# Kernel tuning notes

Hardware: AMD Instinct MI355X
Metric: run time of the kernel (lower is better)

The kernel has to match this reference:

```python
import jax, jax.numpy as jnp
import numpy as np

H = W = 128          # input_size
N = 128              # output_size[0] == output_size[1]
B = 64
LIN = (H - 2) * (W - 2)          # 15876
TRI = (N * N + N) // 2           # 8256
TI, TJ = np.triu_indices(N)
TI = jnp.asarray(TI); TJ = jnp.asarray(TJ)


def setup_inputs() -> dict:
    key = jax.random.key(0)
    ks = jax.random.split(key, 7)
    return {
        "x": jax.random.normal(ks[0], (B, 1, H, W), jnp.float32),
        "conv1_w": jax.random.normal(ks[1], (4, 1, 3, 3), jnp.float32) * 0.1,
        "conv1_b": jax.random.normal(ks[2], (4,), jnp.float32) * 0.1,
        "conv2_w": jax.random.normal(ks[3], (1, 4, 1, 1), jnp.float32) * 0.1,
        "conv2_b": jax.random.normal(ks[4], (1,), jnp.float32) * 0.1,
        "out_w": jax.random.normal(ks[5], (TRI, LIN), jnp.float32) * (1.0 / np.sqrt(LIN)),
        "out_b": jax.random.normal(ks[6], (TRI,), jnp.float32) * 0.01,
    }


def reference(x, conv1_w, conv1_b, conv2_w, conv2_b, out_w, out_b):
    dn = ('NCHW', 'OIHW', 'NCHW')
    # conv1 (1->4, 3x3, VALID) + relu
    h = jax.lax.conv_general_dilated(x, conv1_w, (1, 1), 'VALID', dimension_numbers=dn)
    h = jax.nn.relu(h + conv1_b[None, :, None, None])
    # conv2 (4->1, 1x1)
    h = jax.lax.conv_general_dilated(h, conv2_w, (1, 1), 'VALID', dimension_numbers=dn)
    h = h + conv2_b[None, :, None, None]
    # flatten -> linear
    h = h.reshape(x.shape[0], -1)                       # [B, LIN]
    v = h @ out_w.T + out_b                             # [B, TRI]
    # vectorized symmetric triu scatter (replaces per-sample Python loop)
    y = jnp.zeros((x.shape[0], N, N), v.dtype)
    y = y.at[:, TI, TJ].set(v).at[:, TJ, TI].set(v)
    return y[:, None, :, :]                             # [B, 1, N, N]
```

## Files before the change

kernel.cpp:

```cpp
#include <hip/hip_runtime.h>
#include <hip/hip_bf16.h>

#define H_IN   128
#define W_IN   128
#define B_SZ   64
#define CONV_O 126
#define K_DIM  15876
#define N_TRI  8256
#define N_OUT  128
#define BK     32
#define BN     64
#define NSTEPS 497
#define K8     1988
#define KSPLIT 16

typedef short  short8  __attribute__((ext_vector_type(8)));
typedef float  floatx4 __attribute__((ext_vector_type(4)));

__device__ inline short f2bf(float f) {
    union { __hip_bfloat16 h; short s; } u;
    u.h = __float2bfloat16(f);
    return u.s;
}

__global__ __launch_bounds__(256) void conv_kernel(
    const float* __restrict__ x,
    const float* __restrict__ w1,
    const float* __restrict__ b1,
    const float* __restrict__ w2,
    const float* __restrict__ b2,
    unsigned short* __restrict__ hsw)
{
    int t = blockIdx.x * 256 + threadIdx.x;
    int j  = t & 7;
    int m  = (t >> 3) & 63;
    int k8 = t >> 9;
    int p  = k8 * 8 + j;
    float val = 0.f;
    if (p < K_DIM) {
        int oy = p / CONV_O;
        int ox = p - oy * CONV_O;
        const float* xb = x + m * (H_IN * W_IN) + oy * W_IN + ox;
        float xin[9];
#pragma unroll
        for (int dy = 0; dy < 3; ++dy)
#pragma unroll
            for (int dx = 0; dx < 3; ++dx)
                xin[dy * 3 + dx] = xb[dy * W_IN + dx];
        float acc = b2[0];
#pragma unroll
        for (int c = 0; c < 4; ++c) {
            float s = b1[c];
#pragma unroll
            for (int q = 0; q < 9; ++q) s = fmaf(w1[c * 9 + q], xin[q], s);
            s = fmaxf(s, 0.f);
            acc = fmaf(w2[c], s, acc);
        }
        val = acc;
    }
    hsw[t] = (unsigned short)f2bf(val);
}

__global__ __launch_bounds__(256, 4) void gemm_kernel(
    const unsigned short* __restrict__ hsw,
    const float* __restrict__ w,
    float* __restrict__ v)
{
    __shared__ __align__(16) short Bs[64 * 40];

    const int n0    = blockIdx.x * BN;
    const int split = blockIdx.y;
    const int s0 = (NSTEPS * split) / KSPLIT;
    const int s1 = (NSTEPS * (split + 1)) / KSPLIT;

    const int t    = threadIdx.x;
    const int lane = t & 63;
    const int wv   = t >> 6;
    const int quad = lane >> 4;
    const int l16  = lane & 15;

    const int mh = (wv >> 1) * 32;
    const int nq = (wv & 1) * 32;

    const int brow = t >> 2;
    const int bk   = (t & 3) * 8;

    const int boff0 = (nq + l16) * 40 + quad * 8;
    const int boff1 = (nq + 16 + l16) * 40 + quad * 8;

    floatx4 acc00 = {0.f,0.f,0.f,0.f}, acc01 = {0.f,0.f,0.f,0.f};
    floatx4 acc10 = {0.f,0.f,0.f,0.f}, acc11 = {0.f,0.f,0.f,0.f};

    for (int s = s0; s < s1; ++s) {
        const int k0 = s * BK;

        const float* wp = w + (size_t)(n0 + brow) * K_DIM + k0 + bk;
        float bv[8];
        if (k0 + BK <= K_DIM) {
            float4 x0 = *(const float4*)wp;
            float4 x1 = *(const float4*)(wp + 4);
            bv[0]=x0.x; bv[1]=x0.y; bv[2]=x0.z; bv[3]=x0.w;
            bv[4]=x1.x; bv[5]=x1.y; bv[6]=x1.z; bv[7]=x1.w;
        } else {
#pragma unroll
            for (int q = 0; q < 8; ++q)
                bv[q] = (k0 + bk + q < K_DIM) ? wp[q] : 0.f;
        }
        short8 bs;
#pragma unroll
        for (int q = 0; q < 8; ++q) bs[q] = f2bf(bv[q]);

        __syncthreads();
        *(short8*)(Bs + brow * 40 + bk) = bs;
        __syncthreads();

        const unsigned short* ap = hsw + (size_t)(s * 4 + quad) * (64 * 8);
        short8 a0 = *(const short8*)(ap + (mh + l16) * 8);
        short8 a1 = *(const short8*)(ap + (mh + 16 + l16) * 8);
        short8 b0 = *(const short8*)(Bs + boff0);
        short8 b1 = *(const short8*)(Bs + boff1);

        acc00 = __builtin_amdgcn_mfma_f32_16x16x32_bf16(a0, b0, acc00, 0, 0, 0);
        acc01 = __builtin_amdgcn_mfma_f32_16x16x32_bf16(a0, b1, acc01, 0, 0, 0);
        acc10 = __builtin_amdgcn_mfma_f32_16x16x32_bf16(a1, b0, acc10, 0, 0, 0);
        acc11 = __builtin_amdgcn_mfma_f32_16x16x32_bf16(a1, b1, acc11, 0, 0, 0);
    }

    const int nc = n0 + nq + l16;
#pragma unroll
    for (int r = 0; r < 4; ++r) {
        int m = mh + quad * 4 + r;
        atomicAdd(&v[(size_t)m * N_TRI + nc],              acc00[r]);
        atomicAdd(&v[(size_t)m * N_TRI + nc + 16],         acc01[r]);
        atomicAdd(&v[(size_t)(m + 16) * N_TRI + nc],       acc10[r]);
        atomicAdd(&v[(size_t)(m + 16) * N_TRI + nc + 16],  acc11[r]);
    }
}

__global__ __launch_bounds__(256) void scatter_kernel(
    const float* __restrict__ v,
    const float* __restrict__ out_b,
    float* __restrict__ y)
{
    int t = blockIdx.x * 256 + threadIdx.x;
    int b  = t >> 14;
    int ij = t & 16383;
    int i = ij >> 7, j = ij & 127;
    int ii = min(i, j), jj = max(i, j);
    int tri = ii * N_OUT - ((ii * (ii - 1)) >> 1) + (jj - ii);
    y[t] = v[(size_t)b * N_TRI + tri] + out_b[tri];
}

extern "C" void kernel_launch(void* const* d_in, const int* in_sizes, int n_in,
                              void* d_out, int out_size, void* d_ws, size_t ws_size,
                              hipStream_t stream) {
    const float* x   = (const float*)d_in[0];
    const float* c1w = (const float*)d_in[1];
    const float* c1b = (const float*)d_in[2];
    const float* c2w = (const float*)d_in[3];
    const float* c2b = (const float*)d_in[4];
    const float* ow  = (const float*)d_in[5];
    const float* ob  = (const float*)d_in[6];
    float* y = (float*)d_out;

    unsigned short* hsw = (unsigned short*)d_ws;
    float* v = (float*)((char*)d_ws + (size_t)K8 * 64 * 8 * 2);

    hipMemsetAsync(v, 0, (size_t)B_SZ * N_TRI * sizeof(float), stream);

    conv_kernel<<<(K8 * 64 * 8) / 256, 256, 0, stream>>>(x, c1w, c1b, c2w, c2b, hsw);
    gemm_kernel<<<dim3(N_TRI / BN, KSPLIT), 256, 0, stream>>>(hsw, ow, v);
    scatter_kernel<<<(B_SZ * N_OUT * N_OUT) / 256, 256, 0, stream>>>(v, ob, y);
}
```

Baseline: 730.1 us.

## Double-buffer GEMM B tile with register prefetch and replace atomics with split-K reduce

The GEMM loop now prefetches the next step's fp32 weight slice and activation fragments into registers while the current step computes. It double-buffers the shared B tile so only one barrier per step is needed instead of two. Split-K partials are written with plain stores to a per-split buffer, and a new reduce kernel sums them, replacing the memset and float atomics. This adds about 34 MB of partial-buffer traffic and an extra launch in exchange for removing atomic contention and the sync stalls.

```diff
diff --git a/kernel.cpp b/kernel.cpp
--- a/kernel.cpp
+++ b/kernel.cpp
@@ -64,9 +64,9 @@
 __global__ __launch_bounds__(256, 4) void gemm_kernel(
     const unsigned short* __restrict__ hsw,
     const float* __restrict__ w,
-    float* __restrict__ v)
-{
-    __shared__ __align__(16) short Bs[64 * 40];
+    float* __restrict__ vp)
+{
+    __shared__ __align__(16) short Bs[2][64 * 40];
 
     const int n0    = blockIdx.x * BN;
     const int split = blockIdx.y;
@@ -88,14 +88,17 @@
     const int boff0 = (nq + l16) * 40 + quad * 8;
     const int boff1 = (nq + 16 + l16) * 40 + quad * 8;
 
+    const float* wrow = w + (size_t)(n0 + brow) * K_DIM + bk;
+
     floatx4 acc00 = {0.f,0.f,0.f,0.f}, acc01 = {0.f,0.f,0.f,0.f};
     floatx4 acc10 = {0.f,0.f,0.f,0.f}, acc11 = {0.f,0.f,0.f,0.f};
 
-    for (int s = s0; s < s1; ++s) {
-        const int k0 = s * BK;
-
-        const float* wp = w + (size_t)(n0 + brow) * K_DIM + k0 + bk;
-        float bv[8];
+    float  bv[8];
+    short8 a0n, a1n;
+
+    {
+        const int k0 = s0 * BK;
+        const float* wp = wrow + k0;
         if (k0 + BK <= K_DIM) {
             float4 x0 = *(const float4*)wp;
             float4 x1 = *(const float4*)(wp + 4);
@@ -106,35 +109,77 @@
             for (int q = 0; q < 8; ++q)
                 bv[q] = (k0 + bk + q < K_DIM) ? wp[q] : 0.f;
         }
-        short8 bs;
-#pragma unroll
-        for (int q = 0; q < 8; ++q) bs[q] = f2bf(bv[q]);
-
-        __syncthreads();
-        *(short8*)(Bs + brow * 40 + bk) = bs;
-        __syncthreads();
-
-        const unsigned short* ap = hsw + (size_t)(s * 4 + quad) * (64 * 8);
-        short8 a0 = *(const short8*)(ap + (mh + l16) * 8);
-        short8 a1 = *(const short8*)(ap + (mh + 16 + l16) * 8);
-        short8 b0 = *(const short8*)(Bs + boff0);
-        short8 b1 = *(const short8*)(Bs + boff1);
+        const unsigned short* ap = hsw + (size_t)(s0 * 4 + quad) * (64 * 8);
+        a0n = *(const short8*)(ap + (mh + l16) * 8);
+        a1n = *(const short8*)(ap + (mh + 16 + l16) * 8);
+    }
+
+    int cur = 0;
+    for (int s = s0; s < s1; ++s) {
+        short8 bs8;
+#pragma unroll
+        for (int q = 0; q < 8; ++q) bs8[q] = f2bf(bv[q]);
+        short8 a0 = a0n, a1 = a1n;
+
+        *(short8*)(&Bs[cur][brow * 40 + bk]) = bs8;
+
+        if (s + 1 < s1) {
+            const int k0 = (s + 1) * BK;
+            const float* wp = wrow + k0;
+            if (k0 + BK <= K_DIM) {
+                float4 x0 = *(const float4*)wp;
+                float4 x1 = *(const float4*)(wp + 4);
+                bv[0]=x0.x; bv[1]=x0.y; bv[2]=x0.z; bv[3]=x0.w;
+                bv[4]=x1.x; bv[5]=x1.y; bv[6]=x1.z; bv[7]=x1.w;
+            } else {
+#pragma unroll
+                for (int q = 0; q < 8; ++q)
+                    bv[q] = (k0 + bk + q < K_DIM) ? wp[q] : 0.f;
+            }
+            const unsigned short* ap = hsw + (size_t)((s + 1) * 4 + quad) * (64 * 8);
+            a0n = *(const short8*)(ap + (mh + l16) * 8);
+            a1n = *(const short8*)(ap + (mh + 16 + l16) * 8);
+        }
+
+        asm volatile("s_waitcnt lgkmcnt(0)" ::: "memory");
+        __builtin_amdgcn_s_barrier();
+
+        short8 b0 = *(const short8*)(&Bs[cur][boff0]);
+        short8 b1 = *(const short8*)(&Bs[cur][boff1]);
 
         acc00 = __builtin_amdgcn_mfma_f32_16x16x32_bf16(a0, b0, acc00, 0, 0, 0);
         acc01 = __builtin_amdgcn_mfma_f32_16x16x32_bf16(a0, b1, acc01, 0, 0, 0);
         acc10 = __builtin_amdgcn_mfma_f32_16x16x32_bf16(a1, b0, acc10, 0, 0, 0);
         acc11 = __builtin_amdgcn_mfma_f32_16x16x32_bf16(a1, b1, acc11, 0, 0, 0);
-    }
-
+
+        cur ^= 1;
+    }
+
+    float* vout = vp + (size_t)split * (B_SZ * N_TRI);
     const int nc = n0 + nq + l16;
 #pragma unroll
     for (int r = 0; r < 4; ++r) {
         int m = mh + quad * 4 + r;
-        atomicAdd(&v[(size_t)m * N_TRI + nc],              acc00[r]);
-        atomicAdd(&v[(size_t)m * N_TRI + nc + 16],         acc01[r]);
-        atomicAdd(&v[(size_t)(m + 16) * N_TRI + nc],       acc10[r]);
-        atomicAdd(&v[(size_t)(m + 16) * N_TRI + nc + 16],  acc11[r]);
-    }
+        vout[(size_t)m * N_TRI + nc]             = acc00[r];
+        vout[(size_t)m * N_TRI + nc + 16]        = acc01[r];
+        vout[(size_t)(m + 16) * N_TRI + nc]      = acc10[r];
+        vout[(size_t)(m + 16) * N_TRI + nc + 16] = acc11[r];
+    }
+}
+
+__global__ __launch_bounds__(256) void reduce_kernel(
+    const float* __restrict__ vp,
+    float* __restrict__ v)
+{
+    int t = blockIdx.x * 256 + threadIdx.x;
+    const float4* p = (const float4*)vp + t;
+    float4 s = {0.f, 0.f, 0.f, 0.f};
+#pragma unroll
+    for (int k = 0; k < KSPLIT; ++k) {
+        float4 x = p[(size_t)k * (B_SZ * N_TRI / 4)];
+        s.x += x.x; s.y += x.y; s.z += x.z; s.w += x.w;
+    }
+    ((float4*)v)[t] = s;
 }
 
 __global__ __launch_bounds__(256) void scatter_kernel(
@@ -164,11 +209,11 @@
     float* y = (float*)d_out;
 
     unsigned short* hsw = (unsigned short*)d_ws;
-    float* v = (float*)((char*)d_ws + (size_t)K8 * 64 * 8 * 2);
-
-    hipMemsetAsync(v, 0, (size_t)B_SZ * N_TRI * sizeof(float), stream);
+    float* vp = (float*)((char*)d_ws + (size_t)K8 * 64 * 8 * 2);
+    float* v  = vp + (size_t)KSPLIT * B_SZ * N_TRI;
 
     conv_kernel<<<(K8 * 64 * 8) / 256, 256, 0, stream>>>(x, c1w, c1b, c2w, c2b, hsw);
-    gemm_kernel<<<dim3(N_TRI / BN, KSPLIT), 256, 0, stream>>>(hsw, ow, v);
+    gemm_kernel<<<dim3(N_TRI / BN, KSPLIT), 256, 0, stream>>>(hsw, ow, vp);
+    reduce_kernel<<<(B_SZ * N_TRI / 4) / 256, 256, 0, stream>>>(vp, v);
     scatter_kernel<<<(B_SZ * N_OUT * N_OUT) / 256, 256, 0, stream>>>(v, ob, y);
 }
```

New measurement: 731.7 us. Within noise of the previous version (+0.2%).
